# Kernel tuning notes

Measured on AMD Instinct MI355X. Metric: run time of the kernel, lower is better.

Reference implementation:

```python
import jax, jax.numpy as jnp
import numpy as np

N_NODES = 50000
N_EDGES = 640000
HIDDEN = 128


def setup_inputs() -> dict:
    key = jax.random.key(0)
    ks = jax.random.split(key, 8)
    z = jax.random.normal(ks[0], (N_NODES, HIDDEN), dtype=jnp.float32)
    sources = jax.random.randint(ks[1], (N_EDGES,), 0, N_NODES)
    dists = jax.random.randint(ks[2], (N_EDGES,), 0, N_NODES)
    weights = jax.random.uniform(ks[3], (N_EDGES, 1), dtype=jnp.float32)
    # nn.Linear-style params: W has shape [out, in]; we store transposed [in, out]
    s_msg = 1.0 / np.sqrt(2 * HIDDEN + 1)
    W_msg = jax.random.uniform(ks[4], (2 * HIDDEN + 1, HIDDEN), minval=-s_msg, maxval=s_msg, dtype=jnp.float32)
    b_msg = jax.random.uniform(ks[5], (HIDDEN,), minval=-s_msg, maxval=s_msg, dtype=jnp.float32)
    s_upd = 1.0 / np.sqrt(2 * HIDDEN)
    W_upd = jax.random.uniform(ks[6], (2 * HIDDEN, HIDDEN), minval=-s_upd, maxval=s_upd, dtype=jnp.float32)
    b_upd = jax.random.uniform(ks[7], (HIDDEN,), minval=-s_upd, maxval=s_upd, dtype=jnp.float32)
    return {"z": z, "sources": sources, "dists": dists, "weights": weights,
            "W_msg": W_msg, "b_msg": b_msg, "W_upd": W_upd, "b_upd": b_upd}


def reference(z, sources, dists, weights, W_msg, b_msg, W_upd, b_upd):
    n = z.shape[0]
    # gather -> concat -> message linear: [E, 2h+1] @ [2h+1, h]
    msg_input = jnp.concatenate([z[sources], z[dists], weights], axis=1)
    messages = msg_input @ W_msg + b_msg
    # scatter-amax aggregate into node buffers (empty nodes -> -inf -> 0)
    agg = jax.ops.segment_max(messages, dists, num_segments=n)
    agg = jnp.where(jnp.isinf(agg), 0.0, agg)
    # update linear on [n, 2h]
    return jnp.concatenate([z, agg], axis=1) @ W_upd + b_upd
```

## Files before the change

### kernel.cpp

```cpp
#include <hip/hip_runtime.h>

#define H 128
#define KSLOT 64

typedef __attribute__((ext_vector_type(8))) short bf8;
typedef __attribute__((ext_vector_type(8))) unsigned short u16x8;
typedef __attribute__((ext_vector_type(4))) float f32x4;

__device__ __forceinline__ unsigned short f2bf(float f) {
    unsigned u = __float_as_uint(f);
    return (unsigned short)((u + 0x7FFFu + ((u >> 16) & 1u)) >> 16);
}
__device__ __forceinline__ float bf2f(unsigned short b) {
    return __uint_as_float(((unsigned)b) << 16);
}
__device__ __forceinline__ bf8 pack_bf8_from_f32(const float* p) {
    bf8 r;
#pragma unroll
    for (int i = 0; i < 8; ++i) r[i] = (short)f2bf(p[i]);
    return r;
}

__global__ __launch_bounds__(256) void prep(
    const float* __restrict__ Wmsg, const float* __restrict__ Wupd,
    unsigned short* __restrict__ WmT,
    unsigned short* __restrict__ WuT,
    int* __restrict__ cnt,
    unsigned short* __restrict__ ZS,
    int N)
{
    const int t = blockIdx.x * 256 + threadIdx.x;
    if (t < N) cnt[t] = 0;
    if (t < 16) {
        u16x8 s;
#pragma unroll
        for (int i = 0; i < 8; ++i) s[i] = 0xFF80;
        *(u16x8*)(ZS + (size_t)N * H + t * 8) = s;
    }
    if (t < 256 * H) {
        const int c = t >> 7, k = t & 127;
        WmT[t] = f2bf(Wmsg[(size_t)(k + (c & 128)) * H + (c & 127)]);
    }
    if (t < H * 256) {
        const int c = t >> 8, k = t & 255;
        WuT[t] = f2bf(Wupd[(size_t)k * H + c]);
    }
}

__global__ __launch_bounds__(256) void gemm1(
    const float* __restrict__ z,
    const unsigned short* __restrict__ WmT,
    unsigned short* __restrict__ ZS,
    unsigned short* __restrict__ ZD,
    int N, int ntiles)
{
    const int l = threadIdx.x & 63;
    const int w = threadIdx.x >> 6;
    const int r = l & 15, g = l >> 4;
    const int colbase = w * 64;
    unsigned short* Out = (w < 2) ? ZS : ZD;
    const int outcol = colbase & 127;

    bf8 wf[4][4];
#pragma unroll
    for (int nf = 0; nf < 4; ++nf)
#pragma unroll
        for (int kk = 0; kk < 4; ++kk)
            wf[kk][nf] = *(const bf8*)(WmT + (size_t)(colbase + nf * 16 + r) * H + kk * 32 + g * 8);

    const f32x4 zero = {0.f, 0.f, 0.f, 0.f};
    for (int tt = blockIdx.x; tt < ntiles; tt += gridDim.x) {
        const int row0 = tt * 32;
#pragma unroll
        for (int m = 0; m < 2; ++m) {
            const int node = row0 + m * 16 + r;
            const int rowc = node < N ? node : N - 1;
            bf8 zf[4];
#pragma unroll
            for (int kk = 0; kk < 4; ++kk)
                zf[kk] = pack_bf8_from_f32(z + (size_t)rowc * H + kk * 32 + g * 8);
            f32x4 acc[4] = {zero, zero, zero, zero};
#pragma unroll
            for (int kk = 0; kk < 4; ++kk)
#pragma unroll
                for (int nf = 0; nf < 4; ++nf)
                    acc[nf] = __builtin_amdgcn_mfma_f32_16x16x32_bf16(wf[kk][nf], zf[kk], acc[nf], 0, 0, 0);
            if (node < N) {
#pragma unroll
                for (int nf = 0; nf < 4; ++nf) {
                    ushort4 o;
                    o.x = f2bf(acc[nf][0]); o.y = f2bf(acc[nf][1]);
                    o.z = f2bf(acc[nf][2]); o.w = f2bf(acc[nf][3]);
                    *(ushort4*)(Out + (size_t)node * H + outcol + nf * 16 + g * 4) = o;
                }
            }
        }
    }
}

__global__ __launch_bounds__(256) void scatter_dense(
    const int* __restrict__ src, const int* __restrict__ dst,
    const float* __restrict__ wgt, int* __restrict__ cnt,
    int2* __restrict__ ew, int E)
{
    int e = blockIdx.x * blockDim.x + threadIdx.x;
    if (e < E) {
        const int d = dst[e];
        int p = atomicAdd(&cnt[d], 1);
        if (p < KSLOT) ew[((size_t)d << 6) + p] = make_int2(src[e], __float_as_int(wgt[e]));
    }
}

__global__ __launch_bounds__(256) void aggregate(
    const unsigned short* __restrict__ ZS,
    const unsigned short* __restrict__ ZD,
    unsigned short* __restrict__ Agg,
    const float* __restrict__ bmsg, const float* __restrict__ wrow,
    const int* __restrict__ cnt, const int2* __restrict__ ew, int N)
{
    const int node = blockIdx.x * 4 + (threadIdx.x >> 6);
    if (node >= N) return;
    const int l = threadIdx.x & 63;
    const int sub = l >> 4;
    const int c16 = l & 15;

    const int d = min(cnt[node], KSLOT);
    const int iters = (d + 7) >> 3;

    float wr[8];
    {
        float4 w0 = *(const float4*)(wrow + c16 * 8);
        float4 w1 = *(const float4*)(wrow + c16 * 8 + 4);
        wr[0] = w0.x; wr[1] = w0.y; wr[2] = w0.z; wr[3] = w0.w;
        wr[4] = w1.x; wr[5] = w1.y; wr[6] = w1.z; wr[7] = w1.w;
    }

    const float NINF = -__builtin_inff();
    float m[8];
#pragma unroll
    for (int i = 0; i < 8; ++i) m[i] = NINF;

    const int2* ep = ew + ((size_t)node << 6) + sub;
    for (int j = 0; j < iters; ++j) {
        const int s0 = j * 8 + sub, s1 = s0 + 4;
        int2 e0 = ep[j * 8];
        int2 e1 = ep[j * 8 + 4];
        const int r0 = (s0 < d) ? e0.x : N;
        const int r1 = (s1 < d) ? e1.x : N;
        const float w0 = (s0 < d) ? __int_as_float(e0.y) : 0.f;
        const float w1 = (s1 < d) ? __int_as_float(e1.y) : 0.f;
        u16x8 v0 = *(const u16x8*)(ZS + (size_t)r0 * H + c16 * 8);
        u16x8 v1 = *(const u16x8*)(ZS + (size_t)r1 * H + c16 * 8);
#pragma unroll
        for (int i = 0; i < 8; ++i)
            m[i] = fmaxf(m[i], __builtin_fmaf(w0, wr[i], bf2f((unsigned short)v0[i])));
#pragma unroll
        for (int i = 0; i < 8; ++i)
            m[i] = fmaxf(m[i], __builtin_fmaf(w1, wr[i], bf2f((unsigned short)v1[i])));
    }
#pragma unroll
    for (int i = 0; i < 8; ++i) {
        m[i] = fmaxf(m[i], __shfl_xor(m[i], 16));
        m[i] = fmaxf(m[i], __shfl_xor(m[i], 32));
    }

    if (sub == 0) {
        u16x8 zd = *(const u16x8*)(ZD + (size_t)node * H + c16 * 8);
        float bm[8];
        float4 b0 = *(const float4*)(bmsg + c16 * 8);
        float4 b1 = *(const float4*)(bmsg + c16 * 8 + 4);
        bm[0] = b0.x; bm[1] = b0.y; bm[2] = b0.z; bm[3] = b0.w;
        bm[4] = b1.x; bm[5] = b1.y; bm[6] = b1.z; bm[7] = b1.w;
        u16x8 o;
#pragma unroll
        for (int i = 0; i < 8; ++i) {
            float r = (d > 0) ? (m[i] + bf2f((unsigned short)zd[i]) + bm[i]) : 0.f;
            o[i] = f2bf(r);
        }
        *(u16x8*)(Agg + (size_t)node * H + c16 * 8) = o;
    }
}

__global__ __launch_bounds__(256) void gemm_upd_mfma(
    const float* __restrict__ z,
    const unsigned short* __restrict__ Agg,
    const unsigned short* __restrict__ WuT,
    const float* __restrict__ bupd,
    float* __restrict__ out, int N, int ntiles)
{
    const int l = threadIdx.x & 63;
    const int w = threadIdx.x >> 6;
    const int r = l & 15, g = l >> 4;
    const int colbase = w * 32;

    bf8 wf[8][2];
#pragma unroll
    for (int nf = 0; nf < 2; ++nf)
#pragma unroll
        for (int kk = 0; kk < 8; ++kk)
            wf[kk][nf] = *(const bf8*)(WuT + (size_t)(colbase + nf * 16 + r) * 256 + kk * 32 + g * 8);
    float4 bias[2];
#pragma unroll
    for (int nf = 0; nf < 2; ++nf)
        bias[nf] = *(const float4*)(bupd + colbase + nf * 16 + g * 4);

    const f32x4 zero = {0.f, 0.f, 0.f, 0.f};
    for (int tt = blockIdx.x; tt < ntiles; tt += gridDim.x) {
        const int row0 = tt * 32;
#pragma unroll
        for (int m = 0; m < 2; ++m) {
            const int node = row0 + m * 16 + r;
            const int rowc = node < N ? node : N - 1;
            bf8 zf[8];
#pragma unroll
            for (int kk = 0; kk < 4; ++kk)
                zf[kk] = pack_bf8_from_f32(z + (size_t)rowc * H + kk * 32 + g * 8);
#pragma unroll
            for (int kk = 4; kk < 8; ++kk)
                zf[kk] = *(const bf8*)(Agg + (size_t)rowc * H + (kk - 4) * 32 + g * 8);
            f32x4 acc[2] = {zero, zero};
#pragma unroll
            for (int kk = 0; kk < 8; ++kk)
#pragma unroll
                for (int nf = 0; nf < 2; ++nf)
                    acc[nf] = __builtin_amdgcn_mfma_f32_16x16x32_bf16(wf[kk][nf], zf[kk], acc[nf], 0, 0, 0);
            if (node < N) {
#pragma unroll
                for (int nf = 0; nf < 2; ++nf) {
                    float4 o;
                    o.x = acc[nf][0] + bias[nf].x;
                    o.y = acc[nf][1] + bias[nf].y;
                    o.z = acc[nf][2] + bias[nf].z;
                    o.w = acc[nf][3] + bias[nf].w;
                    *(float4*)(out + (size_t)node * H + colbase + nf * 16 + g * 4) = o;
                }
            }
        }
    }
}

extern "C" void kernel_launch(void* const* d_in, const int* in_sizes, int n_in,
                              void* d_out, int out_size, void* d_ws, size_t ws_size,
                              hipStream_t stream) {
    const float* z    = (const float*)d_in[0];
    const int*   src  = (const int*)d_in[1];
    const int*   dst  = (const int*)d_in[2];
    const float* wgt  = (const float*)d_in[3];
    const float* Wmsg = (const float*)d_in[4];
    const float* bmsg = (const float*)d_in[5];
    const float* Wupd = (const float*)d_in[6];
    const float* bupd = (const float*)d_in[7];
    float* out = (float*)d_out;

    const int N = in_sizes[0] / H;
    const int E = in_sizes[1];
    const int Npad = ((N + 31) / 32) * 32;
    const int ntiles = Npad / 32;

    unsigned short* ZS  = (unsigned short*)d_ws;
    unsigned short* ZD  = ZS + (size_t)(Npad + 32) * H;
    unsigned short* Agg = ZD + (size_t)Npad * H;
    unsigned short* WmT = Agg + (size_t)Npad * H;
    unsigned short* WuT = WmT + 256 * H;
    int*  cnt = (int*)(WuT + H * 256);
    int2* ew  = (int2*)(cnt + ((N + 3) & ~3));

    const int nbN = (N + 255) / 256;
    const int nbE = (E + 255) / 256;

    prep<<<nbN, 256, 0, stream>>>(Wmsg, Wupd, WmT, WuT, cnt, ZS, N);

    gemm1<<<784, 256, 0, stream>>>(z, WmT, ZS, ZD, N, ntiles);

    scatter_dense<<<nbE, 256, 0, stream>>>(src, dst, wgt, cnt, ew, E);

    aggregate<<<(N + 3) / 4, 256, 0, stream>>>(
        ZS, ZD, Agg, bmsg, Wmsg + (size_t)256 * H, cnt, ew, N);

    gemm_upd_mfma<<<784, 256, 0, stream>>>(z, Agg, WuT, bupd, out, N, ntiles);
}
```

Measured before the change: 134.9 us.

## Fuse edge scatter into gemm1 launch and pad per-node counters to 64 bytes

Merges the edge-bucketing scatter into the same launch as the node projection GEMM, using extra blocks that each handle four edges per thread, so the two independent stages overlap and one launch is removed. Per-node atomic counters are padded to a 16-int stride so each node's counter sits on its own 64-byte segment, which is meant to reduce atomic contention between neighbouring nodes. The cost is a larger counter array, wider zeroing in prep, and scattered counter reads in aggregate.

```diff
diff --git a/kernel.cpp b/kernel.cpp
--- a/kernel.cpp
+++ b/kernel.cpp
@@ -2,6 +2,7 @@
 
 #define H 128
 #define KSLOT 64
+#define CSTRIDE 16
 
 typedef __attribute__((ext_vector_type(8))) short bf8;
 typedef __attribute__((ext_vector_type(8))) unsigned short u16x8;
@@ -30,7 +31,8 @@
     int N)
 {
     const int t = blockIdx.x * 256 + threadIdx.x;
-    if (t < N) cnt[t] = 0;
+    const int n4 = (N * CSTRIDE) >> 2;
+    if (t < n4) ((int4*)cnt)[t] = make_int4(0, 0, 0, 0);
     if (t < 16) {
         u16x8 s;
 #pragma unroll
@@ -47,13 +49,36 @@
     }
 }
 
-__global__ __launch_bounds__(256) void gemm1(
+__global__ __launch_bounds__(256) void gemm1_scatter(
     const float* __restrict__ z,
     const unsigned short* __restrict__ WmT,
     unsigned short* __restrict__ ZS,
     unsigned short* __restrict__ ZD,
-    int N, int ntiles)
-{
+    const int* __restrict__ src, const int* __restrict__ dst,
+    const float* __restrict__ wgt, int* __restrict__ cnt,
+    int2* __restrict__ ew,
+    int N, int E, int ntiles, int ngemm)
+{
+    if ((int)blockIdx.x >= ngemm) {
+        const int base = (blockIdx.x - ngemm) * 1024 + threadIdx.x;
+        int dv[4], sv[4]; float wv[4]; bool ok[4];
+#pragma unroll
+        for (int k = 0; k < 4; ++k) {
+            const int e = base + k * 256;
+            ok[k] = e < E;
+            const int ec = ok[k] ? e : 0;
+            dv[k] = dst[ec]; sv[k] = src[ec]; wv[k] = wgt[ec];
+        }
+#pragma unroll
+        for (int k = 0; k < 4; ++k) {
+            if (ok[k]) {
+                int p = atomicAdd(&cnt[(size_t)dv[k] * CSTRIDE], 1);
+                if (p < KSLOT)
+                    ew[((size_t)dv[k] << 6) + p] = make_int2(sv[k], __float_as_int(wv[k]));
+            }
+        }
+        return;
+    }
     const int l = threadIdx.x & 63;
     const int w = threadIdx.x >> 6;
     const int r = l & 15, g = l >> 4;
@@ -69,7 +94,7 @@
             wf[kk][nf] = *(const bf8*)(WmT + (size_t)(colbase + nf * 16 + r) * H + kk * 32 + g * 8);
 
     const f32x4 zero = {0.f, 0.f, 0.f, 0.f};
-    for (int tt = blockIdx.x; tt < ntiles; tt += gridDim.x) {
+    for (int tt = blockIdx.x; tt < ntiles; tt += ngemm) {
         const int row0 = tt * 32;
 #pragma unroll
         for (int m = 0; m < 2; ++m) {
@@ -98,19 +123,6 @@
     }
 }
 
-__global__ __launch_bounds__(256) void scatter_dense(
-    const int* __restrict__ src, const int* __restrict__ dst,
-    const float* __restrict__ wgt, int* __restrict__ cnt,
-    int2* __restrict__ ew, int E)
-{
-    int e = blockIdx.x * blockDim.x + threadIdx.x;
-    if (e < E) {
-        const int d = dst[e];
-        int p = atomicAdd(&cnt[d], 1);
-        if (p < KSLOT) ew[((size_t)d << 6) + p] = make_int2(src[e], __float_as_int(wgt[e]));
-    }
-}
-
 __global__ __launch_bounds__(256) void aggregate(
     const unsigned short* __restrict__ ZS,
     const unsigned short* __restrict__ ZD,
@@ -124,7 +136,7 @@
     const int sub = l >> 4;
     const int c16 = l & 15;
 
-    const int d = min(cnt[node], KSLOT);
+    const int d = min(cnt[(size_t)node * CSTRIDE], KSLOT);
     const int iters = (d + 7) >> 3;
 
     float wr[8];
@@ -263,16 +275,16 @@
     unsigned short* WmT = Agg + (size_t)Npad * H;
     unsigned short* WuT = WmT + 256 * H;
     int*  cnt = (int*)(WuT + H * 256);
-    int2* ew  = (int2*)(cnt + ((N + 3) & ~3));
-
-    const int nbN = (N + 255) / 256;
-    const int nbE = (E + 255) / 256;
-
-    prep<<<nbN, 256, 0, stream>>>(Wmsg, Wupd, WmT, WuT, cnt, ZS, N);
-
-    gemm1<<<784, 256, 0, stream>>>(z, WmT, ZS, ZD, N, ntiles);
-
-    scatter_dense<<<nbE, 256, 0, stream>>>(src, dst, wgt, cnt, ew, E);
+    int2* ew  = (int2*)(cnt + (size_t)N * CSTRIDE);
+
+    const int ngemm = 784;
+    const int nscat = (E + 1023) / 1024;
+    const int nprep = ((N * CSTRIDE / 4) + 255) / 256;
+
+    prep<<<nprep, 256, 0, stream>>>(Wmsg, Wupd, WmT, WuT, cnt, ZS, N);
+
+    gemm1_scatter<<<ngemm + nscat, 256, 0, stream>>>(
+        z, WmT, ZS, ZD, src, dst, wgt, cnt, ew, N, E, ntiles, ngemm);
 
     aggregate<<<(N + 3) / 4, 256, 0, stream>>>(
         ZS, ZD, Agg, bmsg, Wmsg + (size_t)256 * H, cnt, ew, N);
```

Measured after the change: 134.3 us. No clear change (-0.4%).
